# Kernel tuning notes

Measured on AMD Instinct MI355X. Metric: run time of the kernel, lower is better.

The kernel has to match this reference:

```python
import jax, jax.numpy as jnp
import numpy as np

N, E = 100000, 1600000
IN_C, HID, OUT_C = 128, 16, 32
H1, H2 = 8, 8  # heads for conv1/conv2; conv3 has 1 head, concat=False
NEG_SLOPE = 0.2


def setup_inputs() -> dict:
    key = jax.random.key(0)
    ks = jax.random.split(key, 16)
    def p(k, shape, fan_in):
        return jax.random.normal(k, shape, jnp.float32) * (1.0 / np.sqrt(fan_in))
    inp = {
        "x": jax.random.normal(ks[0], (N, IN_C), jnp.float32),
        "edge_index": jax.random.randint(ks[1], (2, E), 0, N, jnp.int32),
        # conv1: in=128 -> heads=8, ch=16, concat
        "W1": p(ks[2], (IN_C, H1 * HID), IN_C),
        "a_src1": p(ks[3], (H1, HID), HID),
        "a_dst1": p(ks[4], (H1, HID), HID),
        "b1": jnp.zeros((H1 * HID,), jnp.float32),
        # conv2: in=128 -> heads=8, ch=16, concat
        "W2": p(ks[5], (H1 * HID, H2 * HID), H1 * HID),
        "a_src2": p(ks[6], (H2, HID), HID),
        "a_dst2": p(ks[7], (H2, HID), HID),
        "b2": jnp.zeros((H2 * HID,), jnp.float32),
        # conv3: in=128 -> heads=1, ch=32, concat=False
        "W3": p(ks[8], (H2 * HID, OUT_C), H2 * HID),
        "a_src3": p(ks[9], (1, OUT_C), OUT_C),
        "a_dst3": p(ks[10], (1, OUT_C), OUT_C),
        "b3": jnp.zeros((OUT_C,), jnp.float32),
    }
    return inp


def gat_conv(x, src, dst, W, a_src, a_dst, b, heads, ch, concat):
    """PyG-style GATConv (eval mode): gather -> leaky_relu -> segment softmax -> scatter sum."""
    n = x.shape[0]
    h = (x @ W).reshape(n, heads, ch)                 # [N, H, C]
    al_s = jnp.sum(h * a_src, axis=-1)                # [N, H] source-side logit part
    al_d = jnp.sum(h * a_dst, axis=-1)                # [N, H] dest-side logit part
    logits = jax.nn.leaky_relu(al_s[src] + al_d[dst], NEG_SLOPE)  # [Etot, H]
    m = jax.ops.segment_max(logits, dst, num_segments=n)         # per-dest max (self loops guarantee >=1 edge)
    e = jnp.exp(logits - m[dst])
    denom = jax.ops.segment_sum(e, dst, num_segments=n)
    alpha = e / denom[dst]                            # [Etot, H]
    msgs = h[src] * alpha[..., None]                  # [Etot, H, C]
    out = jax.ops.segment_sum(msgs, dst, num_segments=n)  # [N, H, C]
    if concat:
        return out.reshape(n, heads * ch) + b
    return out.mean(axis=1) + b


def reference(x, edge_index, W1, a_src1, a_dst1, b1, W2, a_src2, a_dst2, b2,
              W3, a_src3, a_dst3, b3):
    n = x.shape[0]
    loops = jnp.arange(n, dtype=edge_index.dtype)     # PyG add_self_loops=True
    src = jnp.concatenate([edge_index[0], loops])
    dst = jnp.concatenate([edge_index[1], loops])
    h = jax.nn.relu(gat_conv(x, src, dst, W1, a_src1, a_dst1, b1, H1, HID, True))
    h = jax.nn.relu(gat_conv(h, src, dst, W2, a_src2, a_dst2, b2, H2, HID, True))
    h = gat_conv(h, src, dst, W3, a_src3, a_dst3, b3, 1, OUT_C, False)
    # global_mean_pool with all-zero batch vector -> mean over all nodes
    return h.mean(axis=0, keepdims=True)              # [1, OUT_C]
```

## Files before the change

### kernel.cpp

```cpp
#include <hip/hip_runtime.h>


typedef unsigned short bfu;
typedef unsigned char u8;
typedef __attribute__((ext_vector_type(8))) short bf16x8;
typedef __attribute__((ext_vector_type(4))) float f32x4;
typedef __attribute__((ext_vector_type(2))) float f32x2;

constexpr int N_NODES = 100000;
constexpr int E_IN    = 1600000;
constexpr int E_TOT   = E_IN + N_NODES;
constexpr float NEG   = 0.2f;
constexpr int P_XCD   = 8;
constexpr int PSZ     = N_NODES / P_XCD;
constexpr int CAP     = 64;
constexpr int AGG32_B = N_NODES / 32;
constexpr int AGG128_B = N_NODES / 32;
constexpr int GEMM_B  = (N_NODES + 63) / 64;
constexpr int EDGE_B4 = (E_TOT / 4 + 255) / 256;
constexpr int FILL_B  = EDGE_B4 * P_XCD;
constexpr int PREP_ITEMS = 43008;
constexpr int PREP_B  = (PREP_ITEMS + 255) / 256;

__device__ inline bfu f2bf(float f) {
    union { float f; unsigned i; } c; c.f = f;
    unsigned x = c.i;
    return (bfu)((x + 0x7fffu + ((x >> 16) & 1u)) >> 16);
}
__device__ inline u8 f2fp8(float f) {
    return (u8)(__builtin_amdgcn_cvt_pk_fp8_f32(f, f, 0, false) & 0xff);
}


__device__ inline void prep_body(int idx,
        const float* __restrict__ W1, const float* __restrict__ W2,
        const float* __restrict__ W3,
        const float* __restrict__ as1, const float* __restrict__ ad1,
        const float* __restrict__ as2, const float* __restrict__ ad2,
        const float* __restrict__ as3, const float* __restrict__ ad3,
        bfu* __restrict__ WtX1, bfu* __restrict__ WtX2, bfu* __restrict__ WtX3) {
    if (idx < 16384) {
        int k = idx >> 7, n = idx & 127;
        WtX1[n * 128 + k] = f2bf(W1[idx]);
    } else if (idx < 32768) {
        int r = idx - 16384;
        int k = r >> 7, n = r & 127;
        WtX2[n * 128 + k] = f2bf(W2[r]);
    } else if (idx < 36864) {
        int r = idx - 32768;
        int k = r >> 5, n = r & 31;
        WtX3[n * 128 + k] = f2bf(W3[r]);
    } else if (idx < 38912) {
        int r = idx - 36864;
        int sd = r >> 10, rr = r & 1023;
        int h = rr >> 7, k = rr & 127;
        const float* a = sd ? ad1 : as1;
        float v = 0.f;
        #pragma unroll
        for (int c = 0; c < 16; ++c) v += W1[k * 128 + h * 16 + c] * a[h * 16 + c];
        WtX1[(128 + sd * 8 + h) * 128 + k] = f2bf(v);
    } else if (idx < 40960) {
        int r = idx - 38912;
        int sd = r >> 10, rr = r & 1023;
        int h = rr >> 7, k = rr & 127;
        const float* a = sd ? ad2 : as2;
        float v = 0.f;
        #pragma unroll
        for (int c = 0; c < 16; ++c) v += W2[k * 128 + h * 16 + c] * a[h * 16 + c];
        WtX2[(128 + sd * 8 + h) * 128 + k] = f2bf(v);
    } else if (idx < 41216) {
        int r = idx - 40960;
        int sd = r >> 7, k = r & 127;
        const float* a = sd ? ad3 : as3;
        float v = 0.f;
        #pragma unroll
        for (int c = 0; c < 32; ++c) v += W3[k * 32 + c] * a[c];
        WtX3[(32 + sd) * 128 + k] = f2bf(v);
    } else if (idx < 43008) {
        WtX3[34 * 128 + (idx - 41216)] = 0;
    }
}


__global__ __launch_bounds__(256) void fill_prep(const int* __restrict__ ei,
        int* __restrict__ cursor, int* __restrict__ srclist,
        const float* __restrict__ W1, const float* __restrict__ W2,
        const float* __restrict__ W3,
        const float* __restrict__ as1, const float* __restrict__ ad1,
        const float* __restrict__ as2, const float* __restrict__ ad2,
        const float* __restrict__ as3, const float* __restrict__ ad3,
        bfu* __restrict__ WtX1, bfu* __restrict__ WtX2, bfu* __restrict__ WtX3) {
    if (blockIdx.x >= FILL_B) {
        int idx = (blockIdx.x - FILL_B) * 256 + threadIdx.x;
        prep_body(idx, W1, W2, W3, as1, ad1, as2, ad2, as3, ad3, WtX1, WtX2, WtX3);
        return;
    }
    int p = blockIdx.x & 7;
    int b = blockIdx.x >> 3;
    int lo = p * PSZ, hi = lo + PSZ;
    int e0 = (b * 256 + threadIdx.x) * 4;
    if (e0 >= E_TOT) return;
    bool self = e0 >= E_IN;
    int4 d4;
    if (!self) d4 = *(const int4*)&ei[E_IN + e0];
    else { int bb = e0 - E_IN; d4 = make_int4(bb, bb + 1, bb + 2, bb + 3); }
    int dd[4] = {d4.x, d4.y, d4.z, d4.w};
    #pragma unroll
    for (int q = 0; q < 4; ++q) {
        int d = dd[q];
        if (d >= lo && d < hi) {
            int s = self ? (e0 - E_IN + q) : ei[e0 + q];
            int pos = atomicAdd(&cursor[d], 1);
            if (pos < CAP) srclist[d * CAP + pos] = s;
        }
    }
}


__device__ inline bf16x8 ldcvt_f32(const float* p) {
    float4 v0 = *(const float4*)p;
    float4 v1 = *(const float4*)(p + 4);
    bf16x8 a;
    a[0] = (short)f2bf(v0.x); a[1] = (short)f2bf(v0.y);
    a[2] = (short)f2bf(v0.z); a[3] = (short)f2bf(v0.w);
    a[4] = (short)f2bf(v1.x); a[5] = (short)f2bf(v1.y);
    a[6] = (short)f2bf(v1.z); a[7] = (short)f2bf(v1.w);
    return a;
}

template<int NTO, bool F32A>
__global__ __launch_bounds__(256) void gemm_mfma(const void* __restrict__ Xg_,
                                                 const bfu* __restrict__ Wt,
                                                 u8* __restrict__ Y,
                                                 float* __restrict__ als,
                                                 float* __restrict__ ald) {
    constexpr int COUT = NTO * 16;
    int wid  = threadIdx.x >> 6;
    int lane = threadIdx.x & 63;
    int m = lane & 15, quad = lane >> 4;
    int rbase = (blockIdx.x * 4 + wid) * 16;
    if (rbase >= N_NODES) return;
    int rA = rbase + m; if (rA >= N_NODES) rA = N_NODES - 1;

    bf16x8 a0, a1, a2, a3;
    if constexpr (F32A) {
        const float* Ap = (const float*)Xg_ + (size_t)rA * 128 + quad * 8;
        a0 = ldcvt_f32(Ap);
        a1 = ldcvt_f32(Ap + 32);
        a2 = ldcvt_f32(Ap + 64);
        a3 = ldcvt_f32(Ap + 96);
    } else {
        const bfu* Ap = (const bfu*)Xg_ + (size_t)rA * 128 + quad * 8;
        a0 = *(const bf16x8*)(Ap);
        a1 = *(const bf16x8*)(Ap + 32);
        a2 = *(const bf16x8*)(Ap + 64);
        a3 = *(const bf16x8*)(Ap + 96);
    }

    const bfu* Bp = Wt + (size_t)m * 128 + quad * 8;
    f32x4 acc[NTO + 1];
    #pragma unroll
    for (int nt = 0; nt <= NTO; nt++) {
        const bfu* Bn = Bp + nt * 16 * 128;
        f32x4 c = {0.f, 0.f, 0.f, 0.f};
        c = __builtin_amdgcn_mfma_f32_16x16x32_bf16(a0, *(const bf16x8*)(Bn),      c, 0, 0, 0);
        c = __builtin_amdgcn_mfma_f32_16x16x32_bf16(a1, *(const bf16x8*)(Bn + 32), c, 0, 0, 0);
        c = __builtin_amdgcn_mfma_f32_16x16x32_bf16(a2, *(const bf16x8*)(Bn + 64), c, 0, 0, 0);
        c = __builtin_amdgcn_mfma_f32_16x16x32_bf16(a3, *(const bf16x8*)(Bn + 96), c, 0, 0, 0);
        acc[nt] = c;
    }

    #pragma unroll
    for (int nt = 0; nt < NTO; nt++) {
        #pragma unroll
        for (int r = 0; r < 4; r++) {
            int row = rbase + quad * 4 + r;
            if (row < N_NODES)
                Y[(size_t)row * COUT + nt * 16 + m] = f2fp8(acc[nt][r]);
        }
    }
    #pragma unroll
    for (int r = 0; r < 4; r++) {
        int row = rbase + quad * 4 + r;
        if (row >= N_NODES) continue;
        float v = acc[NTO][r];
        if constexpr (NTO == 8) {
            if (m < 8) als[row * 8 + m] = v;
            else       ald[row * 8 + (m - 8)] = v;
        } else {
            if (m == 0) als[row] = v;
            else if (m == 1) ald[row] = v;
        }
    }
}


__device__ inline void unpack_fma(uint4 u, float w, float* a) {
    f32x2 p;
    p = __builtin_amdgcn_cvt_pk_f32_fp8((int)u.x, false); a[0]=fmaf(w,p[0],a[0]);  a[1]=fmaf(w,p[1],a[1]);
    p = __builtin_amdgcn_cvt_pk_f32_fp8((int)u.x, true);  a[2]=fmaf(w,p[0],a[2]);  a[3]=fmaf(w,p[1],a[3]);
    p = __builtin_amdgcn_cvt_pk_f32_fp8((int)u.y, false); a[4]=fmaf(w,p[0],a[4]);  a[5]=fmaf(w,p[1],a[5]);
    p = __builtin_amdgcn_cvt_pk_f32_fp8((int)u.y, true);  a[6]=fmaf(w,p[0],a[6]);  a[7]=fmaf(w,p[1],a[7]);
    p = __builtin_amdgcn_cvt_pk_f32_fp8((int)u.z, false); a[8]=fmaf(w,p[0],a[8]);  a[9]=fmaf(w,p[1],a[9]);
    p = __builtin_amdgcn_cvt_pk_f32_fp8((int)u.z, true);  a[10]=fmaf(w,p[0],a[10]); a[11]=fmaf(w,p[1],a[11]);
    p = __builtin_amdgcn_cvt_pk_f32_fp8((int)u.w, false); a[12]=fmaf(w,p[0],a[12]); a[13]=fmaf(w,p[1],a[13]);
    p = __builtin_amdgcn_cvt_pk_f32_fp8((int)u.w, true);  a[14]=fmaf(w,p[0],a[14]); a[15]=fmaf(w,p[1],a[15]);
}

__global__ __launch_bounds__(256) void agg128(const u8* __restrict__ Hb,
        const float* __restrict__ als, const float* __restrict__ ald,
        const int* __restrict__ deg, const int* __restrict__ srclist,
        const float* __restrict__ bias, bfu* __restrict__ out) {
    int wave = blockIdx.x * 4 + (threadIdx.x >> 6);
    int lane = threadIdx.x & 63;
    int sub  = lane >> 3;
    int li   = lane & 7;
    int d    = wave * 8 + sub;
    int c0   = li * 16;
    float ad = ald[d * 8 + li];
    const int* sl = srclist + d * CAP;
    int n = deg[d]; n = n < CAP ? n : CAP;
    float a[16];
    #pragma unroll
    for (int k = 0; k < 16; ++k) a[k] = 0.f;
    float den = 0.f;
    int j = 0;
    for (; j + 2 <= n; j += 2) {
        int s0 = sl[j], s1 = sl[j + 1];
        uint4 u0 = *(const uint4*)(Hb + (size_t)s0 * 128 + c0);
        uint4 u1 = *(const uint4*)(Hb + (size_t)s1 * 128 + c0);
        float x0 = als[s0 * 8 + li], x1 = als[s1 * 8 + li];
        float l0 = x0 + ad; l0 = fmaxf(l0, NEG * l0); float w0 = __expf(l0);
        float l1 = x1 + ad; l1 = fmaxf(l1, NEG * l1); float w1 = __expf(l1);
        den += w0 + w1;
        unpack_fma(u0, w0, a);
        unpack_fma(u1, w1, a);
    }
    if (j < n) {
        int s0 = sl[j];
        uint4 u0 = *(const uint4*)(Hb + (size_t)s0 * 128 + c0);
        float x0 = als[s0 * 8 + li];
        float l0 = x0 + ad; l0 = fmaxf(l0, NEG * l0); float w0 = __expf(l0);
        den += w0;
        unpack_fma(u0, w0, a);
    }
    float r = 1.f / den;
    unsigned dw[8];
    #pragma unroll
    for (int k = 0; k < 8; ++k) {
        float e0 = fmaxf(fmaf(a[2*k],   r, bias[c0 + 2*k]),   0.f);
        float e1 = fmaxf(fmaf(a[2*k+1], r, bias[c0 + 2*k+1]), 0.f);
        dw[k] = (unsigned)f2bf(e0) | ((unsigned)f2bf(e1) << 16);
    }
    uint4 st0 = {dw[0], dw[1], dw[2], dw[3]};
    uint4 st1 = {dw[4], dw[5], dw[6], dw[7]};
    *(uint4*)&out[(size_t)d * 128 + c0]     = st0;
    *(uint4*)&out[(size_t)d * 128 + c0 + 8] = st1;
}

__global__ __launch_bounds__(256) void agg32(const u8* __restrict__ Hb,
        const float* __restrict__ als, const float* __restrict__ ald,
        const int* __restrict__ deg, const int* __restrict__ srclist,
        const float* __restrict__ bias, float* __restrict__ outp) {
    __shared__ float lds[4][32];
    int t    = threadIdx.x;
    int wid  = t >> 6;
    int lane = t & 63;
    int sub  = lane >> 3;
    int li   = lane & 7;
    int d    = blockIdx.x * 32 + wid * 8 + sub;
    int c0 = li * 4;
    float adv = ald[d];
    const int* sl = srclist + d * CAP;
    int n = deg[d]; n = n < CAP ? n : CAP;
    float a0=0.f,a1=0.f,a2=0.f,a3=0.f,den=0.f;
    int j = 0;
    for (; j + 4 <= n; j += 4) {
        int s0 = sl[j], s1 = sl[j+1], s2 = sl[j+2], s3 = sl[j+3];
        unsigned u0 = *(const unsigned*)(Hb + (size_t)s0 * 32 + c0);
        unsigned u1 = *(const unsigned*)(Hb + (size_t)s1 * 32 + c0);
        unsigned u2 = *(const unsigned*)(Hb + (size_t)s2 * 32 + c0);
        unsigned u3 = *(const unsigned*)(Hb + (size_t)s3 * 32 + c0);
        float x0 = als[s0], x1 = als[s1], x2 = als[s2], x3 = als[s3];
        float l0 = x0 + adv; l0 = fmaxf(l0, NEG*l0); float w0 = __expf(l0);
        float l1 = x1 + adv; l1 = fmaxf(l1, NEG*l1); float w1 = __expf(l1);
        float l2 = x2 + adv; l2 = fmaxf(l2, NEG*l2); float w2 = __expf(l2);
        float l3 = x3 + adv; l3 = fmaxf(l3, NEG*l3); float w3 = __expf(l3);
        den += (w0 + w1) + (w2 + w3);
        f32x2 p;
        p = __builtin_amdgcn_cvt_pk_f32_fp8((int)u0, false); a0=fmaf(w0,p[0],a0); a1=fmaf(w0,p[1],a1);
        p = __builtin_amdgcn_cvt_pk_f32_fp8((int)u0, true);  a2=fmaf(w0,p[0],a2); a3=fmaf(w0,p[1],a3);
        p = __builtin_amdgcn_cvt_pk_f32_fp8((int)u1, false); a0=fmaf(w1,p[0],a0); a1=fmaf(w1,p[1],a1);
        p = __builtin_amdgcn_cvt_pk_f32_fp8((int)u1, true);  a2=fmaf(w1,p[0],a2); a3=fmaf(w1,p[1],a3);
        p = __builtin_amdgcn_cvt_pk_f32_fp8((int)u2, false); a0=fmaf(w2,p[0],a0); a1=fmaf(w2,p[1],a1);
        p = __builtin_amdgcn_cvt_pk_f32_fp8((int)u2, true);  a2=fmaf(w2,p[0],a2); a3=fmaf(w2,p[1],a3);
        p = __builtin_amdgcn_cvt_pk_f32_fp8((int)u3, false); a0=fmaf(w3,p[0],a0); a1=fmaf(w3,p[1],a1);
        p = __builtin_amdgcn_cvt_pk_f32_fp8((int)u3, true);  a2=fmaf(w3,p[0],a2); a3=fmaf(w3,p[1],a3);
    }
    for (; j < n; ++j) {
        int s0 = sl[j];
        unsigned u0 = *(const unsigned*)(Hb + (size_t)s0 * 32 + c0);
        float x0 = als[s0];
        float l0 = x0 + adv; l0 = fmaxf(l0, NEG*l0); float w0 = __expf(l0);
        den += w0;
        f32x2 p;
        p = __builtin_amdgcn_cvt_pk_f32_fp8((int)u0, false); a0=fmaf(w0,p[0],a0); a1=fmaf(w0,p[1],a1);
        p = __builtin_amdgcn_cvt_pk_f32_fp8((int)u0, true);  a2=fmaf(w0,p[0],a2); a3=fmaf(w0,p[1],a3);
    }
    float r = 1.f / den;
    float4 bv = *(const float4*)&bias[c0];
    float o0 = fmaf(a0, r, bv.x), o1 = fmaf(a1, r, bv.y);
    float o2 = fmaf(a2, r, bv.z), o3 = fmaf(a3, r, bv.w);
    #pragma unroll
    for (int mask = 8; mask < 64; mask <<= 1) {
        o0 += __shfl_xor(o0, mask);
        o1 += __shfl_xor(o1, mask);
        o2 += __shfl_xor(o2, mask);
        o3 += __shfl_xor(o3, mask);
    }
    if (sub == 0) {
        lds[wid][c0]     = o0;
        lds[wid][c0 + 1] = o1;
        lds[wid][c0 + 2] = o2;
        lds[wid][c0 + 3] = o3;
    }
    __syncthreads();
    if (t < 32)
        atomicAdd(&outp[t],
            (lds[0][t] + lds[1][t] + lds[2][t] + lds[3][t]) * (1.0f / N_NODES));
}


extern "C" void kernel_launch(void* const* d_in, const int* in_sizes, int n_in,
                              void* d_out, int out_size, void* d_ws, size_t ws_size,
                              hipStream_t stream) {
    (void)in_sizes; (void)n_in; (void)out_size; (void)ws_size;
    const float* x   = (const float*)d_in[0];
    const int*   ei  = (const int*)d_in[1];
    const float* W1  = (const float*)d_in[2];
    const float* as1 = (const float*)d_in[3];
    const float* ad1 = (const float*)d_in[4];
    const float* b1  = (const float*)d_in[5];
    const float* W2  = (const float*)d_in[6];
    const float* as2 = (const float*)d_in[7];
    const float* ad2 = (const float*)d_in[8];
    const float* b2  = (const float*)d_in[9];
    const float* W3  = (const float*)d_in[10];
    const float* as3 = (const float*)d_in[11];
    const float* ad3 = (const float*)d_in[12];
    const float* b3  = (const float*)d_in[13];

    char* ws = (char*)d_ws;
    size_t off = 0;
    auto carve = [&](size_t bytes) { void* p = ws + off; off += (bytes + 255) & ~size_t(255); return p; };
    u8*    bufH    = (u8*)carve(size_t(N_NODES) * 128);
    bfu*   bufF    = (bfu*)carve(size_t(N_NODES) * 128 * 2);
    float* als     = (float*)carve(size_t(N_NODES) * 8 * 4);
    float* ald     = (float*)carve(size_t(N_NODES) * 8 * 4);
    int*   cursor  = (int*)carve(size_t(N_NODES) * 4);
    bfu*   WtX1    = (bfu*)carve(144 * 128 * 2);
    bfu*   WtX2    = (bfu*)carve(144 * 128 * 2);
    bfu*   WtX3    = (bfu*)carve(48 * 128 * 2);
    int*   srclist = (int*)carve(size_t(N_NODES) * CAP * 4);

    hipMemsetAsync(cursor, 0, size_t(N_NODES) * 4, stream);
    hipMemsetAsync(d_out, 0, 32 * 4, stream);

    fill_prep<<<FILL_B + PREP_B, 256, 0, stream>>>(ei, cursor, srclist,
        W1, W2, W3, as1, ad1, as2, ad2, as3, ad3, WtX1, WtX2, WtX3);

    gemm_mfma<8, true><<<GEMM_B, 256, 0, stream>>>(x, WtX1, bufH, als, ald);
    agg128<<<AGG128_B, 256, 0, stream>>>(bufH, als, ald, cursor, srclist, b1, bufF);

    gemm_mfma<8, false><<<GEMM_B, 256, 0, stream>>>(bufF, WtX2, bufH, als, ald);
    agg128<<<AGG128_B, 256, 0, stream>>>(bufH, als, ald, cursor, srclist, b2, bufF);

    gemm_mfma<2, false><<<GEMM_B, 256, 0, stream>>>(bufF, WtX3, bufH, als, ald);
    agg32<<<AGG32_B, 256, 0, stream>>>(bufH, als, ald, cursor, srclist, b3, (float*)d_out);
}
```

Before: 432.7 us.

## Build per-node source lists via two-pass LDS bucket sort instead of global atomics

Replaces the partitioned atomic fill of the adjacency lists with a two-stage scheme. Edges are first binned by destination range into 49 global buckets using shared-memory staging, then a second kernel assembles each 256-node block's source lists in LDS and writes them out coalesced. Self loops are inserted directly, and the per-node capacity shrinks from 64 to 48. This cuts per-edge global atomics and the repeated edge scans, at the cost of an extra kernel, a bucket buffer with a fixed capacity that could overflow, and heavy LDS use in assemble.

```diff
diff --git a/kernel.cpp b/kernel.cpp
--- a/kernel.cpp
+++ b/kernel.cpp
@@ -6,19 +6,20 @@
 typedef __attribute__((ext_vector_type(8))) short bf16x8;
 typedef __attribute__((ext_vector_type(4))) float f32x4;
 typedef __attribute__((ext_vector_type(2))) float f32x2;
+typedef __attribute__((ext_vector_type(4))) int i32x4;
 
 constexpr int N_NODES = 100000;
 constexpr int E_IN    = 1600000;
-constexpr int E_TOT   = E_IN + N_NODES;
 constexpr float NEG   = 0.2f;
-constexpr int P_XCD   = 8;
-constexpr int PSZ     = N_NODES / P_XCD;
-constexpr int CAP     = 64;
+constexpr int CAP     = 48;
 constexpr int AGG32_B = N_NODES / 32;
 constexpr int AGG128_B = N_NODES / 32;
 constexpr int GEMM_B  = (N_NODES + 63) / 64;
-constexpr int EDGE_B4 = (E_TOT / 4 + 255) / 256;
-constexpr int FILL_B  = EDGE_B4 * P_XCD;
+constexpr int NBKT    = 49;
+constexpr int BKCAP   = 34816;
+constexpr int BINCAP  = 64;
+constexpr int BIN_B   = (E_IN / 4 + 255) / 256;
+constexpr int ASM_B   = (N_NODES + 255) / 256;
 constexpr int PREP_ITEMS = 43008;
 constexpr int PREP_B  = (PREP_ITEMS + 255) / 256;
 
@@ -82,38 +83,85 @@
 }
 
 
-__global__ __launch_bounds__(256) void fill_prep(const int* __restrict__ ei,
-        int* __restrict__ cursor, int* __restrict__ srclist,
+__global__ __launch_bounds__(256) void bin_edges(const int* __restrict__ ei,
+        unsigned* __restrict__ gbkt, int* __restrict__ gcount,
         const float* __restrict__ W1, const float* __restrict__ W2,
         const float* __restrict__ W3,
         const float* __restrict__ as1, const float* __restrict__ ad1,
         const float* __restrict__ as2, const float* __restrict__ ad2,
         const float* __restrict__ as3, const float* __restrict__ ad3,
         bfu* __restrict__ WtX1, bfu* __restrict__ WtX2, bfu* __restrict__ WtX3) {
-    if (blockIdx.x >= FILL_B) {
-        int idx = (blockIdx.x - FILL_B) * 256 + threadIdx.x;
+    if (blockIdx.x >= BIN_B) {
+        int idx = (blockIdx.x - BIN_B) * 256 + threadIdx.x;
         prep_body(idx, W1, W2, W3, as1, ad1, as2, ad2, as3, ad3, WtX1, WtX2, WtX3);
         return;
     }
-    int p = blockIdx.x & 7;
-    int b = blockIdx.x >> 3;
-    int lo = p * PSZ, hi = lo + PSZ;
-    int e0 = (b * 256 + threadIdx.x) * 4;
-    if (e0 >= E_TOT) return;
-    bool self = e0 >= E_IN;
-    int4 d4;
-    if (!self) d4 = *(const int4*)&ei[E_IN + e0];
-    else { int bb = e0 - E_IN; d4 = make_int4(bb, bb + 1, bb + 2, bb + 3); }
-    int dd[4] = {d4.x, d4.y, d4.z, d4.w};
-    #pragma unroll
-    for (int q = 0; q < 4; ++q) {
-        int d = dd[q];
-        if (d >= lo && d < hi) {
-            int s = self ? (e0 - E_IN + q) : ei[e0 + q];
-            int pos = atomicAdd(&cursor[d], 1);
-            if (pos < CAP) srclist[d * CAP + pos] = s;
+    __shared__ unsigned bins[NBKT][BINCAP];
+    __shared__ int cnt[NBKT];
+    __shared__ int base[NBKT];
+    int tid = threadIdx.x;
+    for (int i = tid; i < NBKT; i += 256) cnt[i] = 0;
+    __syncthreads();
+    int e0 = (blockIdx.x * 256 + tid) * 4;
+    if (e0 < E_IN) {
+        i32x4 s4 = *(const i32x4*)(ei + e0);
+        i32x4 d4 = *(const i32x4*)(ei + E_IN + e0);
+        #pragma unroll
+        for (int q = 0; q < 4; ++q) {
+            int d = d4[q], s = s4[q];
+            int bkt = d >> 11;
+            unsigned pk = (unsigned)s | ((unsigned)(d & 2047) << 17);
+            int pos = atomicAdd(&cnt[bkt], 1);
+            if (pos < BINCAP) bins[bkt][pos] = pk;
+            else {
+                int gp = atomicAdd(&gcount[bkt], 1);
+                if (gp < BKCAP) gbkt[(size_t)bkt * BKCAP + gp] = pk;
+            }
         }
     }
+    __syncthreads();
+    for (int i = tid; i < NBKT; i += 256) {
+        int c = cnt[i]; c = c < BINCAP ? c : BINCAP;
+        base[i] = atomicAdd(&gcount[i], c);
+        cnt[i] = c;
+    }
+    __syncthreads();
+    for (int b = 0; b < NBKT; ++b) {
+        int c = cnt[b], bs = base[b];
+        for (int i = tid; i < c; i += 256)
+            gbkt[(size_t)b * BKCAP + bs + i] = bins[b][i];
+    }
+}
+
+
+__global__ __launch_bounds__(256) void assemble(const unsigned* __restrict__ gbkt,
+        const int* __restrict__ gcount, int* __restrict__ deg,
+        int* __restrict__ srclist) {
+    __shared__ int sl[256 * CAP];
+    __shared__ int cnt[256];
+    int b = blockIdx.x;
+    int nbase = b * 256;
+    int M = N_NODES - nbase; M = M < 256 ? M : 256;
+    int tid = threadIdx.x;
+    if (tid < M) { cnt[tid] = 1; sl[tid * CAP] = nbase + tid; }
+    __syncthreads();
+    int q = b >> 3;
+    int lo = (b & 7) * 256;
+    int c = gcount[q]; c = c < BKCAP ? c : BKCAP;
+    const unsigned* src = gbkt + (size_t)q * BKCAP;
+    for (int i = tid; i < c; i += 256) {
+        unsigned u = src[i];
+        int rel = (int)(u >> 17) - lo;
+        if ((unsigned)rel < 256u) {
+            int s = (int)(u & 0x1FFFFu);
+            int pos = atomicAdd(&cnt[rel], 1);
+            if (pos < CAP) sl[rel * CAP + pos] = s;
+        }
+    }
+    __syncthreads();
+    if (tid < M) { int cc = cnt[tid]; deg[nbase + tid] = cc < CAP ? cc : CAP; }
+    for (int i = tid * 4; i < M * CAP; i += 1024)
+        *(int4*)&srclist[(size_t)nbase * CAP + i] = *(const int4*)&sl[i];
 }
 
 
@@ -218,8 +266,8 @@
     int d    = wave * 8 + sub;
     int c0   = li * 16;
     float ad = ald[d * 8 + li];
-    const int* sl = srclist + d * CAP;
-    int n = deg[d]; n = n < CAP ? n : CAP;
+    const int* sl = srclist + (size_t)d * CAP;
+    int n = deg[d];
     float a[16];
     #pragma unroll
     for (int k = 0; k < 16; ++k) a[k] = 0.f;
@@ -271,8 +319,8 @@
     int d    = blockIdx.x * 32 + wid * 8 + sub;
     int c0 = li * 4;
     float adv = ald[d];
-    const int* sl = srclist + d * CAP;
-    int n = deg[d]; n = n < CAP ? n : CAP;
+    const int* sl = srclist + (size_t)d * CAP;
+    int n = deg[d];
     float a0=0.f,a1=0.f,a2=0.f,a3=0.f,den=0.f;
     int j = 0;
     for (; j + 4 <= n; j += 4) {
@@ -357,24 +405,27 @@
     bfu*   bufF    = (bfu*)carve(size_t(N_NODES) * 128 * 2);
     float* als     = (float*)carve(size_t(N_NODES) * 8 * 4);
     float* ald     = (float*)carve(size_t(N_NODES) * 8 * 4);
-    int*   cursor  = (int*)carve(size_t(N_NODES) * 4);
+    int*   deg     = (int*)carve(size_t(N_NODES) * 4);
+    int*   gcount  = (int*)carve(NBKT * 4);
     bfu*   WtX1    = (bfu*)carve(144 * 128 * 2);
     bfu*   WtX2    = (bfu*)carve(144 * 128 * 2);
     bfu*   WtX3    = (bfu*)carve(48 * 128 * 2);
     int*   srclist = (int*)carve(size_t(N_NODES) * CAP * 4);
-
-    hipMemsetAsync(cursor, 0, size_t(N_NODES) * 4, stream);
+    unsigned* gbkt = (unsigned*)carve(size_t(NBKT) * BKCAP * 4);
+
+    hipMemsetAsync(gcount, 0, NBKT * 4, stream);
     hipMemsetAsync(d_out, 0, 32 * 4, stream);
 
-    fill_prep<<<FILL_B + PREP_B, 256, 0, stream>>>(ei, cursor, srclist,
+    bin_edges<<<BIN_B + PREP_B, 256, 0, stream>>>(ei, gbkt, gcount,
         W1, W2, W3, as1, ad1, as2, ad2, as3, ad3, WtX1, WtX2, WtX3);
+    assemble<<<ASM_B, 256, 0, stream>>>(gbkt, gcount, deg, srclist);
 
     gemm_mfma<8, true><<<GEMM_B, 256, 0, stream>>>(x, WtX1, bufH, als, ald);
-    agg128<<<AGG128_B, 256, 0, stream>>>(bufH, als, ald, cursor, srclist, b1, bufF);
+    agg128<<<AGG128_B, 256, 0, stream>>>(bufH, als, ald, deg, srclist, b1, bufF);
 
     gemm_mfma<8, false><<<GEMM_B, 256, 0, stream>>>(bufF, WtX2, bufH, als, ald);
-    agg128<<<AGG128_B, 256, 0, stream>>>(bufH, als, ald, cursor, srclist, b2, bufF);
+    agg128<<<AGG128_B, 256, 0, stream>>>(bufH, als, ald, deg, srclist, b2, bufF);
 
     gemm_mfma<2, false><<<GEMM_B, 256, 0, stream>>>(bufF, WtX3, bufH, als, ald);
-    agg32<<<AGG32_B, 256, 0, stream>>>(bufH, als, ald, cursor, srclist, b3, (float*)d_out);
-}
+    agg32<<<AGG32_B, 256, 0, stream>>>(bufH, als, ald, deg, srclist, b3, (float*)d_out);
+}
```

Result: slower. 461.0 us (+6.5%).
